# Performance work log

Hardware: AMD Instinct MI355X
Metric: run time of the kernel (lower is better)

Reference implementation:

```python
import jax, jax.numpy as jnp
import numpy as np

N_NODES = 20000
N_EDGES = 32000
BN_EPS = 1e-5


def _w(key, fan_in, fan_out):
    return jax.random.normal(key, (fan_in, fan_out), jnp.float32) / np.sqrt(fan_in).astype(np.float32)


def setup_inputs() -> dict:
    key = jax.random.key(0)
    ks = jax.random.split(key, 16)
    x = jax.random.normal(ks[0], (N_NODES, 5120), jnp.float32)
    edge_index = jax.random.randint(ks[1], (2, N_EDGES), 0, N_NODES, dtype=jnp.int64)
    return dict(
        x=x,
        W1l=_w(ks[2], 5120, 1680), b1=jnp.zeros((1680,), jnp.float32), W1r=_w(ks[3], 5120, 1680),
        W2l=_w(ks[4], 1680, 640), b2=jnp.zeros((640,), jnp.float32), W2r=_w(ks[5], 1680, 640),
        bn_gamma=jax.random.uniform(ks[6], (1680,), jnp.float32, 0.5, 1.5),
        bn_beta=jax.random.normal(ks[7], (1680,), jnp.float32) * 0.1,
        bn_mean=jnp.zeros((1680,), jnp.float32),
        bn_var=jnp.ones((1680,), jnp.float32),
        lin1_W=_w(ks[8], 640, 320), lin1_b=jnp.zeros((320,), jnp.float32),
        lin2_W=_w(ks[9], 320, 160), lin2_b=jnp.zeros((160,), jnp.float32),
        lin3_W=_w(ks[10], 160, 2), lin3_b=jnp.zeros((2,), jnp.float32),
        edge_index=edge_index,
    )


def _segment_mean(feat, dst, n):
    # mean-aggregate messages feat[e] into their destination node; 0 for isolated nodes (PyG semantics)
    s = jax.ops.segment_sum(feat, dst, num_segments=n)
    cnt = jax.ops.segment_sum(jnp.ones((dst.shape[0],), feat.dtype), dst, num_segments=n)
    return s / jnp.maximum(cnt, 1.0)[:, None]


def reference(x, W1l, b1, W1r, W2l, b2, W2r, bn_gamma, bn_beta, bn_mean, bn_var,
              lin1_W, lin1_b, lin2_W, lin2_b, lin3_W, lin3_b, edge_index):
    src, dst = edge_index[0], edge_index[1]
    n = x.shape[0]
    # SAGEConv 1: lin_l(mean_j x_j) + lin_r(x_i)
    h = _segment_mean(x[src], dst, n) @ W1l + b1 + x @ W1r
    h = jax.nn.relu(h)
    # BatchNorm1d in eval mode (running stats); dropout inactive in eval
    h = (h - bn_mean) * jax.lax.rsqrt(bn_var + BN_EPS) * bn_gamma + bn_beta
    # SAGEConv 2
    h2 = _segment_mean(h[src], dst, n) @ W2l + b2 + h @ W2r
    o = jax.nn.relu(h2)
    o = jax.nn.relu(o @ lin1_W + lin1_b)
    o = jax.nn.relu(o @ lin2_W + lin2_b)
    return o @ lin3_W + lin3_b
```

## Files before the change

kernel.cpp:

```cpp
#include <hip/hip_runtime.h>
#include <stdint.h>

#define NN 20000
#define NE 32000
#define BN_EPS 1e-5f

typedef __attribute__((ext_vector_type(8))) __bf16 bf16x8;
typedef __attribute__((ext_vector_type(4))) float f32x4;
typedef unsigned short u16;
typedef uint32_t u32;

__device__ __forceinline__ u16 f2bf(float f) {
    u32 u = __float_as_uint(f);
    u += 0x7FFFu + ((u >> 16) & 1u);
    return (u16)(u >> 16);
}
__device__ __forceinline__ float bf2f(u16 u) {
    return __uint_as_float(((u32)u) << 16);
}

__device__ __forceinline__ void gload_lds16(const void* g, void* l) {
    __builtin_amdgcn_global_load_lds(
        (const __attribute__((address_space(1))) void*)g,
        (__attribute__((address_space(3))) void*)(uintptr_t)l,
        16, 0, 0);
}

#define LDSRD(base, r, cb) (*(const bf16x8*)((const char*)(base) + (r)*128 + (cb)))

#define DS_A(apb, qm) do { \
  _Pragma("unroll") for (int m4_ = 0; m4_ < 4; ++m4_) { \
    int r_ = (qm)*128 + m4_*32 + wr16 + lrow; \
    aR[m4_][0] = LDSRD(apb, r_, cb0); \
    aR[m4_][1] = LDSRD(apb, r_, cb1); \
  } } while (0)

#define DS_B(bpb, qn) do { \
  _Pragma("unroll") for (int n2_ = 0; n2_ < 2; ++n2_) { \
    int n_ = (qn)*2 + n2_; \
    int r_ = n_*64 + wc16 + lrow; \
    bR[n_][0] = LDSRD(bpb, r_, cb0); \
    bR[n_][1] = LDSRD(bpb, r_, cb1); \
  } } while (0)

#define MM(qm, qn) do { \
  _Pragma("unroll") for (int m4_ = 0; m4_ < 4; ++m4_) \
  _Pragma("unroll") for (int n2_ = 0; n2_ < 2; ++n2_) { \
    int mi_ = (qm)*4 + m4_, ni_ = (qn)*2 + n2_; \
    acc[mi_][ni_] = __builtin_amdgcn_mfma_f32_16x16x32_bf16(aR[m4_][0], bR[ni_][0], acc[mi_][ni_], 0, 0, 0); \
    acc[mi_][ni_] = __builtin_amdgcn_mfma_f32_16x16x32_bf16(aR[m4_][1], bR[ni_][1], acc[mi_][ni_], 0, 0, 0); \
  } } while (0)

#define PHASE_TOP() do { __builtin_amdgcn_s_barrier(); \
  asm volatile("s_waitcnt lgkmcnt(0)" ::: "memory"); \
  __builtin_amdgcn_s_setprio(1); } while (0)
#define PHASE_END() do { __builtin_amdgcn_s_setprio(0); \
  __builtin_amdgcn_s_barrier(); } while (0)
#define PHASE_END_VM() do { __builtin_amdgcn_s_setprio(0); \
  asm volatile("s_waitcnt vmcnt(6)" ::: "memory"); \
  __builtin_amdgcn_s_barrier(); } while (0)

#define KLOOP_BODY(nit_) do { \
  for (int it = 0; it < (nit_); ++it) { \
    const int t1 = 2 * it + 1, t2 = 2 * it + 2, t3 = 2 * it + 3; \
    DS_A(&As[0][0][0], 0); DS_B(&Bs[0][0][0], 0); \
    SA(1, 1, t1); \
    PHASE_TOP(); MM(0, 0); PHASE_END(); \
    DS_B(&Bs[0][0][0], 1); \
    SA(0, 0, t2); \
    PHASE_TOP(); MM(0, 1); PHASE_END(); \
    DS_A(&As[0][0][0], 1); \
    SB(0, 0, t2); \
    PHASE_TOP(); MM(1, 1); PHASE_END(); \
    SB(0, 1, t2); \
    __builtin_amdgcn_s_barrier(); \
    __builtin_amdgcn_s_setprio(1); \
    MM(1, 0); \
    PHASE_END_VM(); \
    DS_A(&As[1][0][0], 0); DS_B(&Bs[1][0][0], 0); \
    SA(0, 1, t2); \
    PHASE_TOP(); MM(0, 0); PHASE_END(); \
    DS_B(&Bs[1][0][0], 1); \
    SA(1, 0, t3); \
    PHASE_TOP(); MM(0, 1); PHASE_END(); \
    DS_A(&As[1][0][0], 1); \
    SB(1, 0, t3); \
    PHASE_TOP(); MM(1, 1); PHASE_END(); \
    SB(1, 1, t3); \
    __builtin_amdgcn_s_barrier(); \
    __builtin_amdgcn_s_setprio(1); \
    MM(1, 0); \
    PHASE_END_VM(); \
  } } while (0)

__global__ __launch_bounds__(512, 2) void gemm1f(
    const u16* __restrict__ xbf, const u16* __restrict__ w1T,
    u16* __restrict__ y1l, u16* __restrict__ y1r,
    const int* __restrict__ clist, const int* __restrict__ nsrcp)
{
    __shared__ __align__(16) u16 As[2][256][64];
    __shared__ __align__(16) u16 Bs[2][256][64];
    const int K = 5120, lda = 5120;
    const int Km64 = K - 64;

    const int nsrc = nsrcp[0];
    const int nmt_l = (nsrc + 255) >> 8;
    const int nl = nmt_l * 7;
    const int nwg = nl + 553;

    int bid = blockIdx.x;
    if (bid >= nwg) return;
    int q8 = nwg >> 3, r8 = nwg & 7;
    int xcd = bid & 7, lid = bid >> 3;
    int wgid = (xcd < r8 ? xcd * (q8 + 1) : r8 * (q8 + 1) + (xcd - r8) * q8) + lid;

    int roleL = (wgid < nl);
    int local, nmt;
    if (roleL) { local = wgid; nmt = nmt_l; }
    else       { local = wgid - nl; nmt = 79; }
    int g = local / 56;
    int first = g << 3;
    int gsz = nmt - first; gsz = gsz < 8 ? gsz : 8;
    int rem = local - g * 56;
    int mt = first + rem % gsz;
    int nt = rem / gsz;

    const int m0 = mt << 8, n0 = nt << 8;
    const int tid = threadIdx.x;
    const int wid = tid >> 6, ln = tid & 63;
    const int wr = wid >> 2, wc = wid & 3;
    const int lrow = ln & 15, khi = ln >> 4;
    const int wr16 = wr << 4, wc16 = wc << 4;
    const int cb0 = (khi << 4) ^ ((lrow & 7) << 4);
    const int cb1 = cb0 ^ 64;
    const int row0 = tid >> 3;
    const int kel = ((tid & 7) ^ (row0 & 7)) << 3;
    const int dstoff = (tid & 448) << 4;

    const u16* Bp = w1T + (roleL ? (size_t)0 : (size_t)1680 * 5120);
    const u16* aB[4];
    const u16* bB[4];
#pragma unroll
    for (int i = 0; i < 4; ++i) {
        int r = m0 + ((i >> 1) << 7) + ((i & 1) << 6) + row0;
        int ga;
        if (roleL) { int idx = r < nsrc ? r : nsrc - 1; ga = clist[idx]; }
        else       { ga = r < NN ? r : NN - 1; }
        aB[i] = xbf + (size_t)ga * lda + kel;
        int rb = n0 + ((i >> 1) << 7) + ((i & 1) << 6) + row0;
        rb = rb < 1680 ? rb : 1679;
        bB[i] = Bp + (size_t)rb * lda + kel;
    }

#define SA(b, ha, t) do { int ks_ = (t) * 64; if (ks_ > Km64) ks_ = Km64; \
  char* d_ = (char*)&As[b][(ha)*128][0] + dstoff; \
  gload_lds16(aB[(ha)*2] + ks_, d_); \
  gload_lds16(aB[(ha)*2 + 1] + ks_, d_ + 8192); } while (0)
#define SB(b, hb, t) do { int ks_ = (t) * 64; if (ks_ > Km64) ks_ = Km64; \
  char* d_ = (char*)&Bs[b][(hb)*128][0] + dstoff; \
  gload_lds16(bB[(hb)*2] + ks_, d_); \
  gload_lds16(bB[(hb)*2 + 1] + ks_, d_ + 8192); } while (0)

    f32x4 acc[8][4];
#pragma unroll
    for (int m = 0; m < 8; ++m)
#pragma unroll
        for (int n = 0; n < 4; ++n)
#pragma unroll
            for (int j = 0; j < 4; ++j) acc[m][n][j] = 0.f;
    bf16x8 aR[4][2], bR[4][2];

    SA(0, 0, 0); SB(0, 0, 0); SB(0, 1, 0); SA(0, 1, 0);
    SA(1, 0, 1); SB(1, 0, 1); SB(1, 1, 1);
    asm volatile("s_waitcnt vmcnt(6)" ::: "memory");
    __builtin_amdgcn_s_barrier();

    KLOOP_BODY(40);

#undef SA
#undef SB

    const int Meff = roleL ? nsrc : NN;
    u16* C = roleL ? y1l : y1r;
#pragma unroll
    for (int m = 0; m < 8; ++m) {
        int gr0 = m0 + m * 32 + wr16 + (khi << 2);
#pragma unroll
        for (int n = 0; n < 4; ++n) {
            int gc = n0 + n * 64 + wc16 + lrow;
            if (gc >= 1680) continue;
#pragma unroll
            for (int j = 0; j < 4; ++j) {
                int gr = gr0 + j;
                if (gr >= Meff) continue;
                C[(size_t)gr * 1680 + gc] = f2bf(acc[m][n][j]);
            }
        }
    }
}

__global__ __launch_bounds__(512, 2) void gemm256(
    const u16* __restrict__ A, const u16* __restrict__ B, u16* __restrict__ C,
    int M, int N, int K, int lda, int ldb, int ldc)
{
    __shared__ __align__(16) u16 As[2][256][64];
    __shared__ __align__(16) u16 Bs[2][256][64];

    const int nmt = (M + 255) >> 8;
    const int ntn = (N + 255) >> 8;
    const int nwg = nmt * ntn;

    int bid = blockIdx.x;
    int q8 = nwg >> 3, r8 = nwg & 7;
    int xcd = bid & 7, lid = bid >> 3;
    int wgid = (xcd < r8 ? xcd * (q8 + 1) : r8 * (q8 + 1) + (xcd - r8) * q8) + lid;
    int per = ntn << 3;
    int g = wgid / per;
    int first = g << 3;
    int gsz = nmt - first; gsz = gsz < 8 ? gsz : 8;
    int rem = wgid - g * per;
    int mt = first + rem % gsz;
    int nt = rem / gsz;

    const int m0 = mt << 8, n0 = nt << 8;
    const int tid = threadIdx.x;
    const int wid = tid >> 6, ln = tid & 63;
    const int wr = wid >> 2, wc = wid & 3;
    const int lrow = ln & 15, khi = ln >> 4;
    const int wr16 = wr << 4, wc16 = wc << 4;
    const int cb0 = (khi << 4) ^ ((lrow & 7) << 4);
    const int cb1 = cb0 ^ 64;
    const int row0 = tid >> 3;
    const int kel = ((tid & 7) ^ (row0 & 7)) << 3;
    const int dstoff = (tid & 448) << 4;
    const int Km64 = K - 64;

#define SA(b, ha, t) do { int ks_ = (t) * 64; if (ks_ > Km64) ks_ = Km64; \
  int ra_ = m0 + (ha)*128 + row0;      ra_ = ra_ < M ? ra_ : M - 1; \
  int rb_ = m0 + (ha)*128 + row0 + 64; rb_ = rb_ < M ? rb_ : M - 1; \
  char* d_ = (char*)&As[b][(ha)*128][0] + dstoff; \
  gload_lds16(A + (size_t)ra_ * lda + ks_ + kel, d_); \
  gload_lds16(A + (size_t)rb_ * lda + ks_ + kel, d_ + 8192); } while (0)
#define SB(b, hb, t) do { int ks_ = (t) * 64; if (ks_ > Km64) ks_ = Km64; \
  int ra_ = n0 + (hb)*128 + row0;      ra_ = ra_ < N ? ra_ : N - 1; \
  int rb_ = n0 + (hb)*128 + row0 + 64; rb_ = rb_ < N ? rb_ : N - 1; \
  char* d_ = (char*)&Bs[b][(hb)*128][0] + dstoff; \
  gload_lds16(B + (size_t)ra_ * ldb + ks_ + kel, d_); \
  gload_lds16(B + (size_t)rb_ * ldb + ks_ + kel, d_ + 8192); } while (0)

    f32x4 acc[8][4];
#pragma unroll
    for (int m = 0; m < 8; ++m)
#pragma unroll
        for (int n = 0; n < 4; ++n)
#pragma unroll
            for (int j = 0; j < 4; ++j) acc[m][n][j] = 0.f;
    bf16x8 aR[4][2], bR[4][2];

    SA(0, 0, 0); SB(0, 0, 0); SB(0, 1, 0); SA(0, 1, 0);
    SA(1, 0, 1); SB(1, 0, 1); SB(1, 1, 1);
    asm volatile("s_waitcnt vmcnt(6)" ::: "memory");
    __builtin_amdgcn_s_barrier();

    const int nit = K >> 7;
    KLOOP_BODY(nit);

#undef SA
#undef SB

#pragma unroll
    for (int m = 0; m < 8; ++m) {
        int gr0 = m0 + m * 32 + wr16 + (khi << 2);
#pragma unroll
        for (int n = 0; n < 4; ++n) {
            int gc = n0 + n * 64 + wc16 + lrow;
            if (gc >= N) continue;
#pragma unroll
            for (int j = 0; j < 4; ++j) {
                int gr = gr0 + j;
                if (gr >= M) continue;
                C[(size_t)gr * ldc + gc] = f2bf(acc[m][n][j]);
            }
        }
    }
}

__global__ void cvt_bf16(const float* __restrict__ in, u16* __restrict__ out, int n4)
{
    for (int i = blockIdx.x * 256 + threadIdx.x; i < n4; i += gridDim.x * 256) {
        float4 v = ((const float4*)in)[i];
        ushort4 o;
        o.x = f2bf(v.x); o.y = f2bf(v.y); o.z = f2bf(v.z); o.w = f2bf(v.w);
        ((ushort4*)out)[i] = o;
    }
}

__device__ __forceinline__ void wtrans_body(
    const float* __restrict__ s0, const float* __restrict__ s1,
    u16* __restrict__ out, int Kin, int Kpad, int N, int nsplit, int kx, int ny)
{
    __shared__ float t[32][33];
    int k0 = kx << 5, n0 = ny << 5;
    int tx = threadIdx.x, ty = threadIdx.y;
#pragma unroll
    for (int i = 0; i < 4; ++i) {
        int k = k0 + ty + (i << 3);
        int n = n0 + tx;
        float v = 0.f;
        if (k < Kin && n < N)
            v = (n < nsplit) ? s0[(size_t)k * nsplit + n]
                             : s1[(size_t)k * (N - nsplit) + (n - nsplit)];
        t[ty + (i << 3)][tx] = v;
    }
    __syncthreads();
#pragma unroll
    for (int i = 0; i < 4; ++i) {
        int n = n0 + ty + (i << 3);
        int k = k0 + tx;
        if (n < N && k < Kpad)
            out[(size_t)n * Kpad + k] = f2bf(t[tx][ty + (i << 3)]);
    }
}

__global__ void wtrans_all(const float* __restrict__ W1l, const float* __restrict__ W1r,
                           const float* __restrict__ l1W, const float* __restrict__ l2W,
                           u16* __restrict__ w1T, u16* __restrict__ l1T, u16* __restrict__ l2T)
{
    int b = blockIdx.x;
    if (b < 16800)
        wtrans_body(W1l, W1r, w1T, 5120, 5120, 3360, 1680, b % 160, b / 160);
    else if (b < 17000) {
        b -= 16800;
        wtrans_body(l1W, l1W, l1T, 640, 640, 320, 320, b % 20, b / 20);
    } else {
        b -= 17000;
        wtrans_body(l2W, l2W, l2T, 320, 320, 160, 160, b % 10, b / 10);
    }
}

__global__ void wtrans_w2(const float* __restrict__ W2l, const float* __restrict__ W2r,
                          u16* __restrict__ w2T)
{
    wtrans_body(W2l, W2r, w2T, 1680, 1792, 1280, 640, blockIdx.x, blockIdx.y);
}

__global__ void deg_mark_k(const int* __restrict__ src, const int* __restrict__ dst,
                           int* __restrict__ deg, int* __restrict__ cmark, int ne)
{
    int e = blockIdx.x * 256 + threadIdx.x;
    if (e < ne) {
        atomicAdd(&deg[dst[e]], 1);
        cmark[src[e]] = 1;
    }
}

__global__ __launch_bounds__(256) void scan2_k(
    const int* __restrict__ deg, int* __restrict__ off, int* __restrict__ cur,
    int* __restrict__ cmark, int* __restrict__ clist, int* __restrict__ nsrcp)
{
    __shared__ int part[256];
    int t = threadIdx.x;
    int st = t * 79;
    int s = 0;
    for (int j = 0; j < 79; ++j) { int i = st + j; if (i < NN) s += deg[i]; }
    part[t] = s;
    __syncthreads();
    for (int d = 1; d < 256; d <<= 1) {
        int v = (t >= d) ? part[t - d] : 0;
        __syncthreads(); part[t] += v; __syncthreads();
    }
    int run = part[t] - s;
    for (int j = 0; j < 79; ++j) {
        int i = st + j;
        if (i < NN) { off[i] = run; cur[i] = run; run += deg[i]; }
    }
    if (t == 255) off[NN] = NE;
    __syncthreads();
    int s2 = 0;
    for (int j = 0; j < 79; ++j) { int i = st + j; if (i < NN) s2 += cmark[i]; }
    part[t] = s2;
    __syncthreads();
    for (int d = 1; d < 256; d <<= 1) {
        int v = (t >= d) ? part[t - d] : 0;
        __syncthreads(); part[t] += v; __syncthreads();
    }
    int run2 = part[t] - s2;
    for (int j = 0; j < 79; ++j) {
        int i = st + j;
        if (i < NN) {
            int m = cmark[i];
            if (m) clist[run2] = i;
            cmark[i] = run2;
            run2 += m;
        }
    }
    if (t == 255) nsrcp[0] = part[255];
}

__global__ void fill_k(const int* __restrict__ src, const int* __restrict__ dst,
                       int* __restrict__ cur, const int* __restrict__ cidx,
                       int* __restrict__ esrc, int ne)
{
    int e = blockIdx.x * 256 + threadIdx.x;
    if (e < ne) {
        int p = atomicAdd(&cur[dst[e]], 1);
        esrc[p] = cidx[src[e]];
    }
}

__global__ __launch_bounds__(256) void agg_bn_k(
    const u16* __restrict__ y1l, const u16* __restrict__ y1r,
    const int* __restrict__ off, const int* __restrict__ esrc,
    const float* __restrict__ b1, const float* __restrict__ gam, const float* __restrict__ bet,
    const float* __restrict__ mn, const float* __restrict__ vr, u16* __restrict__ h)
{
    int b = blockIdx.x, t = threadIdx.x;
    int o0 = off[b], o1 = off[b + 1];
    int deg = o1 - o0;
    int col = t << 3;
    if (t >= 210) {
        if (t < 224) {
            bf16x8 z = (bf16x8)(__bf16)0.f;
            *(bf16x8*)&h[(size_t)b * 1792 + col] = z;
        }
        return;
    }
    float s[8];
#pragma unroll
    for (int i = 0; i < 8; ++i) s[i] = 0.f;
    for (int j = o0; j < o1; ++j) {
        int sc = esrc[j];
        bf16x8 v = *(const bf16x8*)&y1l[(size_t)sc * 1680 + col];
#pragma unroll
        for (int i = 0; i < 8; ++i) s[i] += (float)v[i];
    }
    float inv = 1.f / (deg > 1 ? (float)deg : 1.f);
    bf16x8 yr = *(const bf16x8*)&y1r[(size_t)b * 1680 + col];
    float4 bb0 = *(const float4*)&b1[col],  bb1 = *(const float4*)&b1[col + 4];
    float4 g0  = *(const float4*)&gam[col], g1  = *(const float4*)&gam[col + 4];
    float4 be0 = *(const float4*)&bet[col], be1 = *(const float4*)&bet[col + 4];
    float4 m0  = *(const float4*)&mn[col],  m1  = *(const float4*)&mn[col + 4];
    float4 v0  = *(const float4*)&vr[col],  v1  = *(const float4*)&vr[col + 4];
    float bbv[8] = {bb0.x, bb0.y, bb0.z, bb0.w, bb1.x, bb1.y, bb1.z, bb1.w};
    float gv[8]  = {g0.x,  g0.y,  g0.z,  g0.w,  g1.x,  g1.y,  g1.z,  g1.w};
    float bev[8] = {be0.x, be0.y, be0.z, be0.w, be1.x, be1.y, be1.z, be1.w};
    float mv[8]  = {m0.x,  m0.y,  m0.z,  m0.w,  m1.x,  m1.y,  m1.z,  m1.w};
    float vv[8]  = {v0.x,  v0.y,  v0.z,  v0.w,  v1.x,  v1.y,  v1.z,  v1.w};
    u16 o[8];
#pragma unroll
    for (int i = 0; i < 8; ++i) {
        float tv = fmaxf(s[i] * inv + bbv[i] + (float)yr[i], 0.f);
        tv = (tv - mv[i]) * rsqrtf(vv[i] + BN_EPS) * gv[i] + bev[i];
        o[i] = f2bf(tv);
    }
    *(ushort4*)&h[(size_t)b * 1792 + col]     = *(ushort4*)&o[0];
    *(ushort4*)&h[(size_t)b * 1792 + col + 4] = *(ushort4*)&o[4];
}

__global__ __launch_bounds__(192) void agg_h2_k(
    const u16* __restrict__ y2, const int* __restrict__ off, const int* __restrict__ esrc,
    const int* __restrict__ clist,
    const float* __restrict__ b2, u16* __restrict__ h2)
{
    int b = blockIdx.x, t = threadIdx.x;
    if (t >= 160) return;
    int o0 = off[b], o1 = off[b + 1];
    int deg = o1 - o0;
    float sx = 0.f, sy = 0.f, sz = 0.f, sw = 0.f;
    for (int j = o0; j < o1; ++j) {
        int s = clist[esrc[j]];
        ushort4 v = *(const ushort4*)&y2[(size_t)s * 1280 + (t << 2)];
        sx += bf2f(v.x); sy += bf2f(v.y); sz += bf2f(v.z); sw += bf2f(v.w);
    }
    float inv = 1.f / (deg > 1 ? (float)deg : 1.f);
    int col = t << 2;
    ushort4 yr = *(const ushort4*)&y2[(size_t)b * 1280 + 640 + col];
    float4 bb = *(const float4*)&b2[col];
    ushort4 o;
    o.x = f2bf(fmaxf(sx * inv + bb.x + bf2f(yr.x), 0.f));
    o.y = f2bf(fmaxf(sy * inv + bb.y + bf2f(yr.y), 0.f));
    o.z = f2bf(fmaxf(sz * inv + bb.z + bf2f(yr.z), 0.f));
    o.w = f2bf(fmaxf(sw * inv + bb.w + bf2f(yr.w), 0.f));
    *(ushort4*)&h2[(size_t)b * 640 + col] = o;
}

__global__ __launch_bounds__(256) void mlp_head_k(
    const u16* __restrict__ h2, const u16* __restrict__ l1T, const float* __restrict__ l1b,
    const u16* __restrict__ l2T, const float* __restrict__ l2b,
    const float* __restrict__ l3W, const float* __restrict__ l3b, float* __restrict__ out)
{
    __shared__ __align__(16) u16 h2s[64][648];
    __shared__ __align__(16) u16 o1s[64][328];
    __shared__ __align__(16) u16 o2s[64][168];
    __shared__ float l3s[320];

    const int tid = threadIdx.x;
    const int r0 = blockIdx.x * 64;
    const int wv = tid >> 6, ln = tid & 63;
    const int lrow = ln & 15, khi = ln >> 4;

    for (int j = tid; j < 320; j += 256) l3s[j] = l3W[j];
    for (int c = tid; c < 64 * 80; c += 256) {
        int row = c / 80, c8 = c - row * 80;
        int gr = r0 + row; gr = gr < NN ? gr : NN - 1;
        bf16x8 v = *(const bf16x8*)&h2[(size_t)gr * 640 + c8 * 8];
        *(bf16x8*)&h2s[row][c8 * 8] = v;
    }
    __syncthreads();

    {
        f32x4 a1[4][5];
#pragma unroll
        for (int m = 0; m < 4; ++m)
#pragma unroll
            for (int n = 0; n < 5; ++n)
#pragma unroll
                for (int j = 0; j < 4; ++j) a1[m][n][j] = 0.f;
        const u16* bp[5];
#pragma unroll
        for (int n = 0; n < 5; ++n)
            bp[n] = l1T + (size_t)(wv * 80 + n * 16 + lrow) * 640 + khi * 8;
        bf16x8 bcur[5], bnxt[5];
#pragma unroll
        for (int n = 0; n < 5; ++n) bcur[n] = *(const bf16x8*)(bp[n]);
        for (int ks = 0; ks < 20; ++ks) {
            if (ks < 19) {
#pragma unroll
                for (int n = 0; n < 5; ++n)
                    bnxt[n] = *(const bf16x8*)(bp[n] + (ks + 1) * 32);
            }
            bf16x8 a[4];
            int kb = ks * 32 + khi * 8;
#pragma unroll
            for (int m = 0; m < 4; ++m)
                a[m] = *(const bf16x8*)&h2s[m * 16 + lrow][kb];
#pragma unroll
            for (int m = 0; m < 4; ++m)
#pragma unroll
                for (int n = 0; n < 5; ++n)
                    a1[m][n] = __builtin_amdgcn_mfma_f32_16x16x32_bf16(a[m], bcur[n], a1[m][n], 0, 0, 0);
#pragma unroll
            for (int n = 0; n < 5; ++n) bcur[n] = bnxt[n];
        }
#pragma unroll
        for (int n = 0; n < 5; ++n) {
            int col = wv * 80 + n * 16 + lrow;
            float bb = l1b[col];
#pragma unroll
            for (int m = 0; m < 4; ++m) {
                int rw = m * 16 + khi * 4;
#pragma unroll
                for (int j = 0; j < 4; ++j)
                    o1s[rw + j][col] = f2bf(fmaxf(a1[m][n][j] + bb, 0.f));
            }
        }
    }
    __syncthreads();

    {
        f32x4 a2[10];
#pragma unroll
        for (int n = 0; n < 10; ++n)
#pragma unroll
            for (int j = 0; j < 4; ++j) a2[n][j] = 0.f;
        for (int ks = 0; ks < 10; ++ks) {
            int kb = ks * 32 + khi * 8;
            bf16x8 a = *(const bf16x8*)&o1s[wv * 16 + lrow][kb];
#pragma unroll
            for (int n = 0; n < 10; ++n) {
                bf16x8 b = *(const bf16x8*)&l2T[(size_t)(n * 16 + lrow) * 320 + kb];
                a2[n] = __builtin_amdgcn_mfma_f32_16x16x32_bf16(a, b, a2[n], 0, 0, 0);
            }
        }
#pragma unroll
        for (int n = 0; n < 10; ++n) {
            int col = n * 16 + lrow;
            float bb = l2b[col];
            int rw = wv * 16 + khi * 4;
#pragma unroll
            for (int j = 0; j < 4; ++j)
                o2s[rw + j][col] = f2bf(fmaxf(a2[n][j] + bb, 0.f));
        }
    }
    __syncthreads();

    if (tid < 64) {
        int gr = r0 + tid;
        if (gr < NN) {
            float a0 = l3b[0], a1v = l3b[1];
#pragma unroll
            for (int c8 = 0; c8 < 20; ++c8) {
                bf16x8 v = *(const bf16x8*)&o2s[tid][c8 * 8];
#pragma unroll
                for (int i = 0; i < 8; ++i) {
                    float f = (float)v[i];
                    a0  += f * l3s[(c8 * 8 + i) * 2];
                    a1v += f * l3s[(c8 * 8 + i) * 2 + 1];
                }
            }
            out[(size_t)gr * 2 + 0] = a0;
            out[(size_t)gr * 2 + 1] = a1v;
        }
    }
}

extern "C" void kernel_launch(void* const* d_in, const int* in_sizes, int n_in,
                              void* d_out, int out_size, void* d_ws, size_t ws_size,
                              hipStream_t stream)
{
    const float* x     = (const float*)d_in[0];
    const float* W1l   = (const float*)d_in[1];
    const float* b1    = (const float*)d_in[2];
    const float* W1r   = (const float*)d_in[3];
    const float* W2l   = (const float*)d_in[4];
    const float* b2    = (const float*)d_in[5];
    const float* W2r   = (const float*)d_in[6];
    const float* gam   = (const float*)d_in[7];
    const float* bet   = (const float*)d_in[8];
    const float* bmean = (const float*)d_in[9];
    const float* bvar  = (const float*)d_in[10];
    const float* l1W   = (const float*)d_in[11];
    const float* l1b   = (const float*)d_in[12];
    const float* l2W   = (const float*)d_in[13];
    const float* l2b   = (const float*)d_in[14];
    const float* l3W   = (const float*)d_in[15];
    const float* l3b   = (const float*)d_in[16];
    const int*   ei    = (const int*)d_in[17];
    const int* src = ei, * dst = ei + NE;

    char* ws = (char*)d_ws;
    u16*   y1l  = (u16*)(ws + 0);
    u16*   y1r  = (u16*)(ws + 68000000);
    u16*   y2   = (u16*)(ws + 0);
    u16*   l1T  = (u16*)(ws + 135200000);
    u16*   l2T  = (u16*)(ws + 135700000);
    u16*   xbf  = (u16*)(ws + 136000000);
    u16*   hbuf = (u16*)(ws + 136000000);
    u16*   h2   = (u16*)(ws + 136000000);
    u16*   w1T  = (u16*)(ws + 341000000);
    u16*   w2T  = (u16*)(ws + 341000000);
    int*   deg   = (int*)(ws + 375500000);
    int*   cmark = (int*)(ws + 375580000);
    int*   off   = (int*)(ws + 375660000);
    int*   cur   = (int*)(ws + 375740008);
    int*   clist = (int*)(ws + 375820008);
    int*   esrc  = (int*)(ws + 375900008);
    int*   nsrcp = (int*)(ws + 376028008);

    hipMemsetAsync(deg, 0, 2 * NN * sizeof(int), stream);
    deg_mark_k<<<(NE + 255) / 256, 256, 0, stream>>>(src, dst, deg, cmark, NE);
    scan2_k<<<1, 256, 0, stream>>>(deg, off, cur, cmark, clist, nsrcp);
    fill_k<<<(NE + 255) / 256, 256, 0, stream>>>(src, dst, cur, cmark, esrc, NE);

    cvt_bf16<<<2048, 256, 0, stream>>>(x, xbf, NN * 5120 / 4);
    wtrans_all<<<17050, dim3(32, 8), 0, stream>>>(W1l, W1r, l1W, l2W, w1T, l1T, l2T);

    gemm1f<<<1106, 512, 0, stream>>>(xbf, w1T, y1l, y1r, clist, nsrcp);

    agg_bn_k<<<NN, 256, 0, stream>>>(y1l, y1r, off, esrc, b1, gam, bet, bmean, bvar, hbuf);

    wtrans_w2<<<dim3(56, 40), dim3(32, 8), 0, stream>>>(W2l, W2r, w2T);

    gemm256<<<79 * 5, 512, 0, stream>>>(hbuf, w2T, y2, NN, 1280, 1792, 1792, 1792, 1280);

    agg_h2_k<<<NN, 192, 0, stream>>>(y2, off, esrc, clist, b2, h2);

    mlp_head_k<<<313, 256, 0, stream>>>(h2, l1T, l1b, l2T, l2b, l3W, l3b, (float*)d_out);
}
```

Measured before the change: 1.063 ms.

## Merge small kernels into co-launched prep, GEMM, aggregation and head kernels

The bf16 conversion of x is merged with the weight transposes into one prep kernel. The CSR edge fill moves into spare workgroups of the first GEMM grid. The W2 transpose rides along with the first aggregation/BN kernel, and the second aggregation is fused into the MLP head so h2 is built directly in LDS. This cuts kernel launches and a global round trip for h2. In exchange, the head kernel now does its gather with only 256 threads per 64 nodes, which may be slower. The edge fill also now depends on the GEMM grid having enough spare blocks.

```diff
diff --git a/kernel.cpp b/kernel.cpp
--- a/kernel.cpp
+++ b/kernel.cpp
@@ -96,7 +96,9 @@
 __global__ __launch_bounds__(512, 2) void gemm1f(
     const u16* __restrict__ xbf, const u16* __restrict__ w1T,
     u16* __restrict__ y1l, u16* __restrict__ y1r,
-    const int* __restrict__ clist, const int* __restrict__ nsrcp)
+    const int* __restrict__ clist, const int* __restrict__ nsrcp,
+    const int* __restrict__ src, const int* __restrict__ dst,
+    int* __restrict__ cur, const int* __restrict__ cidx, int* __restrict__ esrc)
 {
     __shared__ __align__(16) u16 As[2][256][64];
     __shared__ __align__(16) u16 Bs[2][256][64];
@@ -109,7 +111,15 @@
     const int nwg = nl + 553;
 
     int bid = blockIdx.x;
-    if (bid >= nwg) return;
+    const int tid = threadIdx.x;
+    if (bid >= nwg) {
+        int nd = 1120 - nwg;
+        for (int e = (bid - nwg) * 512 + tid; e < NE; e += nd * 512) {
+            int p = atomicAdd(&cur[dst[e]], 1);
+            esrc[p] = cidx[src[e]];
+        }
+        return;
+    }
     int q8 = nwg >> 3, r8 = nwg & 7;
     int xcd = bid & 7, lid = bid >> 3;
     int wgid = (xcd < r8 ? xcd * (q8 + 1) : r8 * (q8 + 1) + (xcd - r8) * q8) + lid;
@@ -126,7 +136,6 @@
     int nt = rem / gsz;
 
     const int m0 = mt << 8, n0 = nt << 8;
-    const int tid = threadIdx.x;
     const int wid = tid >> 6, ln = tid & 63;
     const int wr = wid >> 2, wc = wid & 3;
     const int lrow = ln & 15, khi = ln >> 4;
@@ -285,23 +294,13 @@
     }
 }
 
-__global__ void cvt_bf16(const float* __restrict__ in, u16* __restrict__ out, int n4)
-{
-    for (int i = blockIdx.x * 256 + threadIdx.x; i < n4; i += gridDim.x * 256) {
-        float4 v = ((const float4*)in)[i];
-        ushort4 o;
-        o.x = f2bf(v.x); o.y = f2bf(v.y); o.z = f2bf(v.z); o.w = f2bf(v.w);
-        ((ushort4*)out)[i] = o;
-    }
-}
-
 __device__ __forceinline__ void wtrans_body(
     const float* __restrict__ s0, const float* __restrict__ s1,
     u16* __restrict__ out, int Kin, int Kpad, int N, int nsplit, int kx, int ny)
 {
     __shared__ float t[32][33];
     int k0 = kx << 5, n0 = ny << 5;
-    int tx = threadIdx.x, ty = threadIdx.y;
+    int tx = threadIdx.x & 31, ty = threadIdx.x >> 5;
 #pragma unroll
     for (int i = 0; i < 4; ++i) {
         int k = k0 + ty + (i << 3);
@@ -322,26 +321,30 @@
     }
 }
 
-__global__ void wtrans_all(const float* __restrict__ W1l, const float* __restrict__ W1r,
-                           const float* __restrict__ l1W, const float* __restrict__ l2W,
-                           u16* __restrict__ w1T, u16* __restrict__ l1T, u16* __restrict__ l2T)
+__global__ __launch_bounds__(256) void prep_k(
+    const float* __restrict__ x, u16* __restrict__ xbf,
+    const float* __restrict__ W1l, const float* __restrict__ W1r,
+    const float* __restrict__ l1W, const float* __restrict__ l2W,
+    u16* __restrict__ w1T, u16* __restrict__ l1T, u16* __restrict__ l2T)
 {
     int b = blockIdx.x;
-    if (b < 16800)
+    if (b < 16800) {
         wtrans_body(W1l, W1r, w1T, 5120, 5120, 3360, 1680, b % 160, b / 160);
-    else if (b < 17000) {
+    } else if (b < 17000) {
         b -= 16800;
         wtrans_body(l1W, l1W, l1T, 640, 640, 320, 320, b % 20, b / 20);
-    } else {
+    } else if (b < 17050) {
         b -= 17000;
         wtrans_body(l2W, l2W, l2T, 320, 320, 160, 160, b % 10, b / 10);
-    }
-}
-
-__global__ void wtrans_w2(const float* __restrict__ W2l, const float* __restrict__ W2r,
-                          u16* __restrict__ w2T)
-{
-    wtrans_body(W2l, W2r, w2T, 1680, 1792, 1280, 640, blockIdx.x, blockIdx.y);
+    } else {
+        const int n4 = NN * 5120 / 4;
+        for (int i = (b - 17050) * 256 + threadIdx.x; i < n4; i += 2048 * 256) {
+            float4 v = ((const float4*)x)[i];
+            ushort4 o;
+            o.x = f2bf(v.x); o.y = f2bf(v.y); o.z = f2bf(v.z); o.w = f2bf(v.w);
+            ((ushort4*)xbf)[i] = o;
+        }
+    }
 }
 
 __global__ void deg_mark_k(const int* __restrict__ src, const int* __restrict__ dst,
@@ -397,24 +400,19 @@
     if (t == 255) nsrcp[0] = part[255];
 }
 
-__global__ void fill_k(const int* __restrict__ src, const int* __restrict__ dst,
-                       int* __restrict__ cur, const int* __restrict__ cidx,
-                       int* __restrict__ esrc, int ne)
-{
-    int e = blockIdx.x * 256 + threadIdx.x;
-    if (e < ne) {
-        int p = atomicAdd(&cur[dst[e]], 1);
-        esrc[p] = cidx[src[e]];
-    }
-}
-
-__global__ __launch_bounds__(256) void agg_bn_k(
+__global__ __launch_bounds__(256) void agg_bn_w2_k(
     const u16* __restrict__ y1l, const u16* __restrict__ y1r,
     const int* __restrict__ off, const int* __restrict__ esrc,
     const float* __restrict__ b1, const float* __restrict__ gam, const float* __restrict__ bet,
-    const float* __restrict__ mn, const float* __restrict__ vr, u16* __restrict__ h)
+    const float* __restrict__ mn, const float* __restrict__ vr, u16* __restrict__ h,
+    const float* __restrict__ W2l, const float* __restrict__ W2r, u16* __restrict__ w2T)
 {
     int b = blockIdx.x, t = threadIdx.x;
+    if (b >= NN) {
+        int bb = b - NN;
+        wtrans_body(W2l, W2r, w2T, 1680, 1792, 1280, 640, bb % 56, bb / 56);
+        return;
+    }
     int o0 = off[b], o1 = off[b + 1];
     int deg = o1 - o0;
     int col = t << 3;
@@ -457,35 +455,10 @@
     *(ushort4*)&h[(size_t)b * 1792 + col + 4] = *(ushort4*)&o[4];
 }
 
-__global__ __launch_bounds__(192) void agg_h2_k(
+__global__ __launch_bounds__(256) void mlp_head_k(
     const u16* __restrict__ y2, const int* __restrict__ off, const int* __restrict__ esrc,
-    const int* __restrict__ clist,
-    const float* __restrict__ b2, u16* __restrict__ h2)
-{
-    int b = blockIdx.x, t = threadIdx.x;
-    if (t >= 160) return;
-    int o0 = off[b], o1 = off[b + 1];
-    int deg = o1 - o0;
-    float sx = 0.f, sy = 0.f, sz = 0.f, sw = 0.f;
-    for (int j = o0; j < o1; ++j) {
-        int s = clist[esrc[j]];
-        ushort4 v = *(const ushort4*)&y2[(size_t)s * 1280 + (t << 2)];
-        sx += bf2f(v.x); sy += bf2f(v.y); sz += bf2f(v.z); sw += bf2f(v.w);
-    }
-    float inv = 1.f / (deg > 1 ? (float)deg : 1.f);
-    int col = t << 2;
-    ushort4 yr = *(const ushort4*)&y2[(size_t)b * 1280 + 640 + col];
-    float4 bb = *(const float4*)&b2[col];
-    ushort4 o;
-    o.x = f2bf(fmaxf(sx * inv + bb.x + bf2f(yr.x), 0.f));
-    o.y = f2bf(fmaxf(sy * inv + bb.y + bf2f(yr.y), 0.f));
-    o.z = f2bf(fmaxf(sz * inv + bb.z + bf2f(yr.z), 0.f));
-    o.w = f2bf(fmaxf(sw * inv + bb.w + bf2f(yr.w), 0.f));
-    *(ushort4*)&h2[(size_t)b * 640 + col] = o;
-}
-
-__global__ __launch_bounds__(256) void mlp_head_k(
-    const u16* __restrict__ h2, const u16* __restrict__ l1T, const float* __restrict__ l1b,
+    const int* __restrict__ clist, const float* __restrict__ b2,
+    const u16* __restrict__ l1T, const float* __restrict__ l1b,
     const u16* __restrict__ l2T, const float* __restrict__ l2b,
     const float* __restrict__ l3W, const float* __restrict__ l3b, float* __restrict__ out)
 {
@@ -500,11 +473,31 @@
     const int lrow = ln & 15, khi = ln >> 4;
 
     for (int j = tid; j < 320; j += 256) l3s[j] = l3W[j];
-    for (int c = tid; c < 64 * 80; c += 256) {
-        int row = c / 80, c8 = c - row * 80;
-        int gr = r0 + row; gr = gr < NN ? gr : NN - 1;
-        bf16x8 v = *(const bf16x8*)&h2[(size_t)gr * 640 + c8 * 8];
-        *(bf16x8*)&h2s[row][c8 * 8] = v;
+
+    {
+        int node = tid >> 2, l4 = tid & 3;
+        int gr = r0 + node; if (gr >= NN) gr = NN - 1;
+        int o0 = off[gr], o1e = off[gr + 1];
+        int deg = o1e - o0;
+        float inv = 1.f / (deg > 1 ? (float)deg : 1.f);
+        for (int i = 0; i < 40; ++i) {
+            int cc = l4 + (i << 2);
+            int col = cc << 2;
+            float sx = 0.f, sy = 0.f, sz = 0.f, sw = 0.f;
+            for (int j = o0; j < o1e; ++j) {
+                int s = clist[esrc[j]];
+                ushort4 v = *(const ushort4*)&y2[(size_t)s * 1280 + col];
+                sx += bf2f(v.x); sy += bf2f(v.y); sz += bf2f(v.z); sw += bf2f(v.w);
+            }
+            ushort4 yr = *(const ushort4*)&y2[(size_t)gr * 1280 + 640 + col];
+            float4 bb = *(const float4*)&b2[col];
+            ushort4 o;
+            o.x = f2bf(fmaxf(sx * inv + bb.x + bf2f(yr.x), 0.f));
+            o.y = f2bf(fmaxf(sy * inv + bb.y + bf2f(yr.y), 0.f));
+            o.z = f2bf(fmaxf(sz * inv + bb.z + bf2f(yr.z), 0.f));
+            o.w = f2bf(fmaxf(sw * inv + bb.w + bf2f(yr.w), 0.f));
+            *(ushort4*)&h2s[node][col] = o;
+        }
     }
     __syncthreads();
 
@@ -636,7 +629,6 @@
     u16*   l2T  = (u16*)(ws + 135700000);
     u16*   xbf  = (u16*)(ws + 136000000);
     u16*   hbuf = (u16*)(ws + 136000000);
-    u16*   h2   = (u16*)(ws + 136000000);
     u16*   w1T  = (u16*)(ws + 341000000);
     u16*   w2T  = (u16*)(ws + 341000000);
     int*   deg   = (int*)(ws + 375500000);
@@ -650,20 +642,17 @@
     hipMemsetAsync(deg, 0, 2 * NN * sizeof(int), stream);
     deg_mark_k<<<(NE + 255) / 256, 256, 0, stream>>>(src, dst, deg, cmark, NE);
     scan2_k<<<1, 256, 0, stream>>>(deg, off, cur, cmark, clist, nsrcp);
-    fill_k<<<(NE + 255) / 256, 256, 0, stream>>>(src, dst, cur, cmark, esrc, NE);
-
-    cvt_bf16<<<2048, 256, 0, stream>>>(x, xbf, NN * 5120 / 4);
-    wtrans_all<<<17050, dim3(32, 8), 0, stream>>>(W1l, W1r, l1W, l2W, w1T, l1T, l2T);
-
-    gemm1f<<<1106, 512, 0, stream>>>(xbf, w1T, y1l, y1r, clist, nsrcp);
-
-    agg_bn_k<<<NN, 256, 0, stream>>>(y1l, y1r, off, esrc, b1, gam, bet, bmean, bvar, hbuf);
-
-    wtrans_w2<<<dim3(56, 40), dim3(32, 8), 0, stream>>>(W2l, W2r, w2T);
+
+    prep_k<<<19098, 256, 0, stream>>>(x, xbf, W1l, W1r, l1W, l2W, w1T, l1T, l2T);
+
+    gemm1f<<<1120, 512, 0, stream>>>(xbf, w1T, y1l, y1r, clist, nsrcp,
+                                     src, dst, cur, cmark, esrc);
+
+    agg_bn_w2_k<<<NN + 2240, 256, 0, stream>>>(y1l, y1r, off, esrc, b1, gam, bet,
+                                               bmean, bvar, hbuf, W2l, W2r, w2T);
 
     gemm256<<<79 * 5, 512, 0, stream>>>(hbuf, w2T, y2, NN, 1280, 1792, 1792, 1792, 1280);
 
-    agg_h2_k<<<NN, 192, 0, stream>>>(y2, off, esrc, clist, b2, h2);
-
-    mlp_head_k<<<313, 256, 0, stream>>>(h2, l1T, l1b, l2T, l2b, l3W, l3b, (float*)d_out);
-}
+    mlp_head_k<<<313, 256, 0, stream>>>(y2, off, esrc, clist, b2,
+                                        l1T, l1b, l2T, l2b, l3W, l3b, (float*)d_out);
+}
```

Result: slower. 1.219 ms (+14.7%).
